# Performance work log

Measured on AMD Instinct MI355X. Metric: run time of the kernel, lower is better.

## Reference

```python
import jax, jax.numpy as jnp
import numpy as np

DIM = 5120
HEADS = 40
HEAD_DIM = DIM // HEADS
EPS = 1e-6


def rms_norm(x, w, eps=EPS):
    var = jnp.mean(jnp.square(x), axis=-1, keepdims=True)
    return x * jax.lax.rsqrt(var + eps) * w


def apply_rotary(x, freqs_cos, freqs_sin):
    # x: [B, L, H, D]; freqs: [1, L, 1, D] (broadcastable)
    x_even = x[..., 0::2]
    x_odd = x[..., 1::2]
    cos_e = freqs_cos[..., 0::2]
    sin_o = freqs_sin[..., 1::2]
    out_even = x_even * cos_e - x_odd * sin_o
    out_odd = x_even * sin_o + x_odd * cos_e
    # interleave back: [..., D//2, 2] -> [..., D]
    return jnp.stack([out_even, out_odd], axis=-1).reshape(x.shape)


def setup_inputs() -> dict:
    key = jax.random.key(0)
    ks = jax.random.split(key, 8)
    B, L = 1, 2048
    scale_in = 1.0 / np.sqrt(DIM)
    return {
        "hidden_states": jax.random.normal(ks[0], (B, L, DIM), jnp.float32),
        "freqs_cos": jax.random.normal(ks[1], (1, L, 1, HEAD_DIM), jnp.float32),
        "freqs_sin": jax.random.normal(ks[2], (1, L, 1, HEAD_DIM), jnp.float32),
        "W_qkv": jax.random.normal(ks[3], (DIM, 3 * DIM), jnp.float32) * scale_in,
        "b_qkv": jnp.zeros((3 * DIM,), jnp.float32),
        "w_norm_q": jnp.ones((DIM,), jnp.float32),
        "w_norm_k": jnp.ones((DIM,), jnp.float32),
        "W_out": jax.random.normal(ks[4], (DIM, DIM), jnp.float32) * scale_in,
        "b_out": jnp.zeros((DIM,), jnp.float32),
    }


def reference(hidden_states, freqs_cos, freqs_sin, W_qkv, b_qkv,
              w_norm_q, w_norm_k, W_out, b_out):
    B, L, D = hidden_states.shape
    qkv = hidden_states @ W_qkv + b_qkv                     # [B, L, 3D]
    q, k, v = jnp.split(qkv, 3, axis=-1)
    q = rms_norm(q, w_norm_q)                               # norm over full dim=5120
    k = rms_norm(k, w_norm_k)
    q = q.reshape(B, L, HEADS, HEAD_DIM)
    k = k.reshape(B, L, HEADS, HEAD_DIM)
    v = v.reshape(B, L, HEADS, HEAD_DIM)
    q = apply_rotary(q, freqs_cos, freqs_sin)
    k = apply_rotary(k, freqs_cos, freqs_sin)
    scale = 1.0 / np.sqrt(HEAD_DIM)
    scores = jnp.einsum("bqhd,bkhd->bhqk", q, k) * scale    # [B, H, L, L]
    attn = jax.nn.softmax(scores, axis=-1)
    out = jnp.einsum("bhqk,bkhd->bqhd", attn, v)            # [B, L, H, D]
    out = out.reshape(B, L, D)
    return out @ W_out + b_out
```

## Files before the change

### kernel.cpp

```cpp
#include <hip/hip_runtime.h>
#include <cstdint>
#include <cstddef>

#define L_C   2048
#define DIMC  5120
#define HD    128
#define NHEADS 40

typedef __bf16 bf16_t;
typedef __bf16 bf16x8 __attribute__((ext_vector_type(8)));
typedef __bf16 bf16x4 __attribute__((ext_vector_type(4)));
typedef float  f32x4  __attribute__((ext_vector_type(4)));

#define MFMA16(A,B,C) __builtin_amdgcn_mfma_f32_16x16x32_bf16((A),(B),(C),0,0,0)
#define BARRIER() __builtin_amdgcn_s_barrier()
#define VMCNT0() asm volatile("s_waitcnt vmcnt(0)" ::: "memory")
#define VMCNT8() asm volatile("s_waitcnt vmcnt(8)" ::: "memory")

__device__ __forceinline__ void gload16(const void* g, void* l) {
  __builtin_amdgcn_global_load_lds(
      (__attribute__((address_space(1))) void*)(void*)g,
      (__attribute__((address_space(3))) void*)l, 16, 0, 0);
}

__global__ __launch_bounds__(256) void f32_to_bf16(const float* __restrict__ in,
                                                   bf16_t* __restrict__ out, size_t n8) {
  size_t i = (size_t)blockIdx.x * blockDim.x + threadIdx.x;
  size_t stride = (size_t)gridDim.x * blockDim.x;
  for (; i < n8; i += stride) {
    f32x4 a = *(const f32x4*)(in + i * 8);
    f32x4 b = *(const f32x4*)(in + i * 8 + 4);
    bf16x8 o;
#pragma unroll
    for (int j = 0; j < 4; ++j) { o[j] = (bf16_t)a[j]; o[4 + j] = (bf16_t)b[j]; }
    *(bf16x8*)(out + i * 8) = o;
  }
}

__global__ __launch_bounds__(256) void wtrans(const float* __restrict__ W,
                                              bf16_t* __restrict__ Wt, int K, int N) {
  __shared__ bf16_t t[64 * 68];
  const int k0 = blockIdx.x * 64, n0 = blockIdx.y * 64, tid = threadIdx.x;
  const int tn = tid & 15, tk = tid >> 4;
  f32x4 v[4];
#pragma unroll
  for (int jj = 0; jj < 4; ++jj)
    v[jj] = *(const f32x4*)(W + (size_t)(k0 + 4 * tk + jj) * N + n0 + 4 * tn);
#pragma unroll
  for (int j = 0; j < 4; ++j) {
    bf16x4 o;
#pragma unroll
    for (int jj = 0; jj < 4; ++jj) o[jj] = (bf16_t)v[jj][j];
    *(bf16x4*)&t[(4 * tn + j) * 68 + 4 * tk] = o;
  }
  __syncthreads();
#pragma unroll
  for (int i = 0; i < 2; ++i) {
    int c = i * 256 + tid, rn = c >> 3, ck = (c & 7) * 8;
    bf16x8 o = *(const bf16x8*)&t[rn * 68 + ck];
    *(bf16x8*)(Wt + (size_t)(n0 + rn) * K + k0 + ck) = o;
  }
}

__global__ __launch_bounds__(256) void v_trans(const bf16_t* __restrict__ qkv,
                                               bf16_t* __restrict__ Vt) {
  __shared__ bf16_t t[128 * 68];
  const int l0 = blockIdx.x * 64, h = blockIdx.y, tid = threadIdx.x;
  const int td = tid & 31, tl = tid >> 5;
#pragma unroll
  for (int it = 0; it < 2; ++it) {
    const int lq = tl + it * 8;
    bf16x4 v[4];
#pragma unroll
    for (int jj = 0; jj < 4; ++jj)
      v[jj] = *(const bf16x4*)(qkv + (size_t)(l0 + 4 * lq + jj) * (3 * DIMC) +
                               2 * DIMC + h * HD + 4 * td);
#pragma unroll
    for (int j = 0; j < 4; ++j) {
      bf16x4 o;
#pragma unroll
      for (int jj = 0; jj < 4; ++jj) o[jj] = v[jj][j];
      *(bf16x4*)&t[(4 * td + j) * 68 + 4 * lq] = o;
    }
  }
  __syncthreads();
#pragma unroll
  for (int i = 0; i < 4; ++i) {
    int c = i * 256 + tid, d = c >> 3, cl = (c & 7) * 8;
    bf16x8 o = *(const bf16x8*)&t[d * 68 + cl];
    *(bf16x8*)(Vt + ((size_t)h * HD + d) * L_C + l0 + cl) = o;
  }
}

template <int OUT_BF16, int K>
__global__ __launch_bounds__(512, 1) void gemm8(const bf16_t* __restrict__ A,
                                                const bf16_t* __restrict__ Bt,
                                                const float* __restrict__ bias,
                                                bf16_t* __restrict__ Cb,
                                                float* __restrict__ Cf,
                                                int M, int N) {
  __shared__ __align__(16) char smem[131072];
  const int tid = threadIdx.x;
  const int wid = tid >> 6, lane = tid & 63;
  const int g = lane >> 4, r = lane & 15;
  const int wm = wid >> 2, wn = wid & 3;
  const int nb = gridDim.x * gridDim.y;
  const int bid = blockIdx.y * gridDim.x + blockIdx.x;
  const int swz = (bid & 7) * (nb >> 3) + (bid >> 3);
  const int bm = swz % gridDim.x, bn = swz / gridDim.x;
  const int row0 = bm * 256, col0 = bn * 256;

  auto stageA = [&](int buf, int half, int kt) {
#pragma unroll
    for (int i = 0; i < 2; ++i) {
      const int idx = i * 512 + tid;
      const int rl = idx >> 3, c = idx & 7;
      gload16(A + (size_t)(row0 + half * 128 + rl) * K + kt * 64 + ((c ^ (rl & 7)) << 3),
              smem + buf * 65536 + half * 16384 + (i * 512 + wid * 64) * 16);
    }
  };
  auto stageB = [&](int buf, int half, int kt) {
#pragma unroll
    for (int i = 0; i < 2; ++i) {
      const int idx = i * 512 + tid;
      const int rl = idx >> 3, c = idx & 7;
      gload16(Bt + (size_t)(col0 + half * 128 + rl) * K + kt * 64 + ((c ^ (rl & 7)) << 3),
              smem + buf * 65536 + 32768 + half * 16384 + (i * 512 + wid * 64) * 16);
    }
  };
  auto ldA = [&](int buf, int mi, int kk) {
    const int rh = mi * 16 + r;
    return *(const bf16x8*)(smem + buf * 65536 + wm * 16384 + rh * 128 +
                            (((kk * 4 + g) ^ (r & 7)) << 4));
  };
  auto ldB = [&](int buf, int ni, int kk) {
    const int rh = (wn & 1) * 64 + ni * 16 + r;
    return *(const bf16x8*)(smem + buf * 65536 + 32768 + (wn >> 1) * 16384 + rh * 128 +
                            (((kk * 4 + g) ^ (r & 7)) << 4));
  };

  f32x4 acc[8][4] = {};
  bf16x8 af[4][2], bfr[4][2];
  constexpr int nk = K / 64;

  stageA(0, 0, 0); stageA(0, 1, 0); stageB(0, 0, 0); stageB(0, 1, 0);
  stageA(1, 0, 1); stageA(1, 1, 1); stageB(1, 0, 1); stageB(1, 1, 1);
  VMCNT8();
  BARRIER();

  auto ktile = [&](int k, int cur) {
    const bool pf2 = (k + 2 < nk);
#pragma unroll
    for (int i = 0; i < 4; ++i)
#pragma unroll
      for (int kk = 0; kk < 2; ++kk) af[i][kk] = ldA(cur, i, kk);
#pragma unroll
    for (int j = 0; j < 2; ++j)
#pragma unroll
      for (int kk = 0; kk < 2; ++kk) bfr[j][kk] = ldB(cur, j, kk);
    BARRIER();
    __builtin_amdgcn_s_setprio(1);
#pragma unroll
    for (int i = 0; i < 4; ++i)
#pragma unroll
      for (int j = 0; j < 2; ++j)
#pragma unroll
        for (int kk = 0; kk < 2; ++kk)
          acc[i][j] = MFMA16(af[i][kk], bfr[j][kk], acc[i][j]);
    __builtin_amdgcn_s_setprio(0);
    BARRIER();
#pragma unroll
    for (int j = 0; j < 2; ++j)
#pragma unroll
      for (int kk = 0; kk < 2; ++kk) bfr[2 + j][kk] = ldB(cur, 2 + j, kk);
    BARRIER();
    __builtin_amdgcn_s_setprio(1);
#pragma unroll
    for (int i = 0; i < 4; ++i)
#pragma unroll
      for (int j = 0; j < 2; ++j)
#pragma unroll
        for (int kk = 0; kk < 2; ++kk)
          acc[i][2 + j] = MFMA16(af[i][kk], bfr[2 + j][kk], acc[i][2 + j]);
    __builtin_amdgcn_s_setprio(0);
    BARRIER();
#pragma unroll
    for (int i = 0; i < 4; ++i)
#pragma unroll
      for (int kk = 0; kk < 2; ++kk) af[i][kk] = ldA(cur, 4 + i, kk);
    if (pf2) { stageB(cur, 0, k + 2); stageB(cur, 1, k + 2); }
    BARRIER();
    __builtin_amdgcn_s_setprio(1);
#pragma unroll
    for (int i = 0; i < 4; ++i)
#pragma unroll
      for (int j = 0; j < 2; ++j)
#pragma unroll
        for (int kk = 0; kk < 2; ++kk)
          acc[4 + i][2 + j] = MFMA16(af[i][kk], bfr[2 + j][kk], acc[4 + i][2 + j]);
    __builtin_amdgcn_s_setprio(0);
    BARRIER();
    if (pf2) { stageA(cur, 0, k + 2); stageA(cur, 1, k + 2); }
    __builtin_amdgcn_s_setprio(1);
#pragma unroll
    for (int i = 0; i < 4; ++i)
#pragma unroll
      for (int j = 0; j < 2; ++j)
#pragma unroll
        for (int kk = 0; kk < 2; ++kk)
          acc[4 + i][j] = MFMA16(af[i][kk], bfr[j][kk], acc[4 + i][j]);
    __builtin_amdgcn_s_setprio(0);
    if (pf2) { VMCNT8(); } else { VMCNT0(); }
    BARRIER();
  };

  for (int kp = 0; kp < nk; kp += 2) { ktile(kp, 0); ktile(kp + 1, 1); }

#pragma unroll
  for (int mi = 0; mi < 8; ++mi)
#pragma unroll
    for (int ni = 0; ni < 4; ++ni)
#pragma unroll
      for (int p = 0; p < 4; ++p) {
        const int rr = row0 + wm * 128 + mi * 16 + 4 * g + p;
        const int cc = col0 + wn * 64 + ni * 16 + r;
        const float v = acc[mi][ni][p] + bias[cc];
        if (OUT_BF16) Cb[(size_t)rr * N + cc] = (bf16_t)v;
        else          Cf[(size_t)rr * N + cc] = v;
      }
}

__global__ __launch_bounds__(256) void norm_rope(const bf16_t* __restrict__ qkv,
                                                 const float* __restrict__ wq,
                                                 const float* __restrict__ wk,
                                                 const float* __restrict__ fcos,
                                                 const float* __restrict__ fsin,
                                                 bf16_t* __restrict__ Qo,
                                                 bf16_t* __restrict__ Ko) {
  __shared__ bf16_t qs[DIMC], ks_[DIMC];
  const int l = blockIdx.x, tid = threadIdx.x;
  const bf16_t* row = qkv + (size_t)l * (3 * DIMC);
  float sq = 0.f, sk = 0.f;
  for (int i = tid; i < DIMC / 8; i += 256) {
    bf16x8 a = *(const bf16x8*)(row + i * 8);
    bf16x8 b = *(const bf16x8*)(row + DIMC + i * 8);
    *(bf16x8*)&qs[i * 8] = a;
    *(bf16x8*)&ks_[i * 8] = b;
#pragma unroll
    for (int j = 0; j < 8; ++j) {
      float x = (float)a[j]; sq += x * x;
      float y = (float)b[j]; sk += y * y;
    }
  }
#pragma unroll
  for (int off = 32; off; off >>= 1) {
    sq += __shfl_xor(sq, off, 64);
    sk += __shfl_xor(sk, off, 64);
  }
  __shared__ float red[2][4];
  const int wid = tid >> 6, lane = tid & 63;
  if (!lane) { red[0][wid] = sq; red[1][wid] = sk; }
  __syncthreads();
  sq = red[0][0] + red[0][1] + red[0][2] + red[0][3];
  sk = red[1][0] + red[1][1] + red[1][2] + red[1][3];
  const float rq = rsqrtf(sq * (1.f / DIMC) + 1e-6f);
  const float rk = rsqrtf(sk * (1.f / DIMC) + 1e-6f);
  for (int i = tid; i < DIMC / 8; i += 256) {
    const int j0 = i * 8, h = j0 >> 7, d0 = j0 & 127;
    bf16x8 a = *(const bf16x8*)&qs[j0];
    bf16x8 b = *(const bf16x8*)&ks_[j0];
    f32x4 cA = *(const f32x4*)(fcos + (size_t)l * HD + d0);
    f32x4 cB = *(const f32x4*)(fcos + (size_t)l * HD + d0 + 4);
    f32x4 sA = *(const f32x4*)(fsin + (size_t)l * HD + d0);
    f32x4 sB = *(const f32x4*)(fsin + (size_t)l * HD + d0 + 4);
    f32x4 wqA = *(const f32x4*)(wq + j0), wqB = *(const f32x4*)(wq + j0 + 4);
    f32x4 wkA = *(const f32x4*)(wk + j0), wkB = *(const f32x4*)(wk + j0 + 4);
    float cc[8], ss[8], qn[8], kn[8];
#pragma unroll
    for (int j = 0; j < 4; ++j) {
      cc[j] = cA[j]; cc[4 + j] = cB[j];
      ss[j] = sA[j]; ss[4 + j] = sB[j];
      qn[j] = (float)a[j] * rq * wqA[j];
      qn[4 + j] = (float)a[4 + j] * rq * wqB[j];
      kn[j] = (float)b[j] * rk * wkA[j];
      kn[4 + j] = (float)b[4 + j] * rk * wkB[j];
    }
    bf16x8 oq, ok;
#pragma unroll
    for (int p = 0; p < 4; ++p) {
      const float c = cc[2 * p], s = ss[2 * p + 1];
      oq[2 * p]     = (bf16_t)(qn[2 * p] * c - qn[2 * p + 1] * s);
      oq[2 * p + 1] = (bf16_t)(qn[2 * p] * s + qn[2 * p + 1] * c);
      ok[2 * p]     = (bf16_t)(kn[2 * p] * c - kn[2 * p + 1] * s);
      ok[2 * p + 1] = (bf16_t)(kn[2 * p] * s + kn[2 * p + 1] * c);
    }
    *(bf16x8*)(Qo + ((size_t)h * L_C + l) * HD + d0) = oq;
    *(bf16x8*)(Ko + ((size_t)h * L_C + l) * HD + d0) = ok;
  }
}

__global__ __launch_bounds__(256, 2) void attn(const bf16_t* __restrict__ Q,
                                               const bf16_t* __restrict__ Kg,
                                               const bf16_t* __restrict__ Vt,
                                               bf16_t* __restrict__ O) {
  __shared__ bf16_t k_lds[64 * HD];
  __shared__ bf16_t v_lds[HD * 64];
  __shared__ bf16_t p_lds[4][2][16 * 72];
  const int tid = threadIdx.x, wid = tid >> 6, lane = tid & 63;
  const int g = lane >> 4, r = lane & 15;
  const int bid = blockIdx.x;
  const int grp = bid & 7, inner = bid >> 3;
  const int h = (inner >> 4) * 8 + grp;
  const int q0 = (inner & 15) * 128 + wid * 32;
  bf16x8 qf[2][4];
#pragma unroll
  for (int rg = 0; rg < 2; ++rg) {
    const bf16_t* qrow = Q + ((size_t)h * L_C + q0 + rg * 16 + r) * HD;
#pragma unroll
    for (int ks = 0; ks < 4; ++ks) qf[rg][ks] = *(const bf16x8*)(qrow + ks * 32 + g * 8);
  }
  f32x4 oacc[2][8] = {};
  float m_i[2][4], l_i[2][4];
#pragma unroll
  for (int rg = 0; rg < 2; ++rg)
#pragma unroll
    for (int p = 0; p < 4; ++p) { m_i[rg][p] = -1e30f; l_i[rg][p] = 0.f; }
  const float scale = 0.08838834764831845f;

  bf16x8 kreg[4], vreg[4];
  auto load_kv = [&](int kv0) {
#pragma unroll
    for (int i = 0; i < 4; ++i) {
      const int c = i * 256 + tid;
      const int krow = c >> 4, kcb = c & 15;
      kreg[i] = *(const bf16x8*)(Kg + ((size_t)h * L_C + kv0 + krow) * HD + kcb * 8);
      const int vrow = c >> 3, vcb = c & 7;
      vreg[i] = *(const bf16x8*)(Vt + ((size_t)h * HD + vrow) * L_C + kv0 + vcb * 8);
    }
  };
  load_kv(0);

  for (int kv0 = 0; kv0 < L_C; kv0 += 64) {
    __syncthreads();
#pragma unroll
    for (int i = 0; i < 4; ++i) {
      const int c = i * 256 + tid;
      const int krow = c >> 4, kcb = c & 15;
      *(bf16x8*)((char*)k_lds + krow * 256 + ((kcb * 16) ^ ((krow & 7) << 4))) = kreg[i];
      const int vrow = c >> 3, vcb = c & 7;
      *(bf16x8*)((char*)v_lds + vrow * 128 + ((vcb * 16) ^ ((vrow & 7) << 4))) = vreg[i];
    }
    if (kv0 + 64 < L_C) load_kv(kv0 + 64);
    __syncthreads();

    float pv[2][4][4];
    __builtin_amdgcn_s_setprio(1);
#pragma unroll
    for (int nf = 0; nf < 4; ++nf) {
      f32x4 s0 = {0.f, 0.f, 0.f, 0.f}, s1 = {0.f, 0.f, 0.f, 0.f};
      const int key = nf * 16 + r;
#pragma unroll
      for (int ks = 0; ks < 4; ++ks) {
        bf16x8 kf = *(const bf16x8*)((const char*)k_lds + key * 256 +
                                     ((ks * 64 + g * 16) ^ ((key & 7) << 4)));
        s0 = MFMA16(qf[0][ks], kf, s0);
        s1 = MFMA16(qf[1][ks], kf, s1);
      }
#pragma unroll
      for (int p = 0; p < 4; ++p) { pv[0][nf][p] = s0[p] * scale; pv[1][nf][p] = s1[p] * scale; }
    }
    __builtin_amdgcn_s_setprio(0);
#pragma unroll
    for (int rg = 0; rg < 2; ++rg) {
      float mnew[4];
#pragma unroll
      for (int p = 0; p < 4; ++p)
        mnew[p] = fmaxf(fmaxf(pv[rg][0][p], pv[rg][1][p]), fmaxf(pv[rg][2][p], pv[rg][3][p]));
#pragma unroll
      for (int m = 1; m < 16; m <<= 1)
#pragma unroll
        for (int p = 0; p < 4; ++p) mnew[p] = fmaxf(mnew[p], __shfl_xor(mnew[p], m, 64));
      float alpha[4], rsum[4];
#pragma unroll
      for (int p = 0; p < 4; ++p) {
        const float mi = fmaxf(m_i[rg][p], mnew[p]);
        alpha[p] = __expf(m_i[rg][p] - mi);
        m_i[rg][p] = mi;
        rsum[p] = 0.f;
      }
#pragma unroll
      for (int nf = 0; nf < 4; ++nf)
#pragma unroll
        for (int p = 0; p < 4; ++p) {
          pv[rg][nf][p] = __expf(pv[rg][nf][p] - m_i[rg][p]);
          rsum[p] += pv[rg][nf][p];
        }
#pragma unroll
      for (int nf = 0; nf < 4; ++nf)
#pragma unroll
        for (int p = 0; p < 4; ++p)
          p_lds[wid][rg][(4 * g + p) * 72 + nf * 16 + r] = (bf16_t)pv[rg][nf][p];
#pragma unroll
      for (int m = 1; m < 16; m <<= 1)
#pragma unroll
        for (int p = 0; p < 4; ++p) rsum[p] += __shfl_xor(rsum[p], m, 64);
#pragma unroll
      for (int p = 0; p < 4; ++p) l_i[rg][p] = l_i[rg][p] * alpha[p] + rsum[p];
#pragma unroll
      for (int nf = 0; nf < 8; ++nf)
#pragma unroll
        for (int p = 0; p < 4; ++p) oacc[rg][nf][p] *= alpha[p];
    }
    bf16x8 pf0[2], pf1[2];
#pragma unroll
    for (int rg = 0; rg < 2; ++rg) {
      pf0[rg] = *(const bf16x8*)&p_lds[wid][rg][r * 72 + 8 * g];
      pf1[rg] = *(const bf16x8*)&p_lds[wid][rg][r * 72 + 32 + 8 * g];
    }
    __builtin_amdgcn_s_setprio(1);
#pragma unroll
    for (int nf = 0; nf < 8; ++nf) {
      const int d = nf * 16 + r;
      bf16x8 vf0 = *(const bf16x8*)((const char*)v_lds + d * 128 +
                                    ((g * 16) ^ ((d & 7) << 4)));
      bf16x8 vf1 = *(const bf16x8*)((const char*)v_lds + d * 128 +
                                    ((64 + g * 16) ^ ((d & 7) << 4)));
#pragma unroll
      for (int rg = 0; rg < 2; ++rg) {
        oacc[rg][nf] = MFMA16(pf0[rg], vf0, oacc[rg][nf]);
        oacc[rg][nf] = MFMA16(pf1[rg], vf1, oacc[rg][nf]);
      }
    }
    __builtin_amdgcn_s_setprio(0);
  }
#pragma unroll
  for (int rg = 0; rg < 2; ++rg)
#pragma unroll
    for (int p = 0; p < 4; ++p) {
      const float inv = 1.f / l_i[rg][p];
      const int rowg = q0 + rg * 16 + 4 * g + p;
#pragma unroll
      for (int nf = 0; nf < 8; ++nf) {
        const int d = nf * 16 + r;
        O[(size_t)rowg * DIMC + h * HD + d] = (bf16_t)(oacc[rg][nf][p] * inv);
      }
    }
}

extern "C" void kernel_launch(void* const* d_in, const int* in_sizes, int n_in,
                              void* d_out, int out_size, void* d_ws, size_t ws_size,
                              hipStream_t stream) {
  const float* hidden = (const float*)d_in[0];
  const float* fcos   = (const float*)d_in[1];
  const float* fsin   = (const float*)d_in[2];
  const float* Wqkv   = (const float*)d_in[3];
  const float* bqkv   = (const float*)d_in[4];
  const float* wnq    = (const float*)d_in[5];
  const float* wnk    = (const float*)d_in[6];
  const float* Wout   = (const float*)d_in[7];
  const float* bout   = (const float*)d_in[8];
  float* out = (float*)d_out;

  char* ws = (char*)d_ws;
  size_t off = 0;
  auto alloc = [&](size_t bytes) {
    void* p = ws + off;
    off += (bytes + 255) & ~(size_t)255;
    return p;
  };
  bf16_t* X   = (bf16_t*)alloc((size_t)L_C * DIMC * 2);
  bf16_t* WQT = (bf16_t*)alloc((size_t)3 * DIMC * DIMC * 2);
  bf16_t* WOT = (bf16_t*)alloc((size_t)DIMC * DIMC * 2);
  bf16_t* QKV = (bf16_t*)alloc((size_t)L_C * 3 * DIMC * 2);
  bf16_t* Qb  = (bf16_t*)alloc((size_t)L_C * DIMC * 2);
  bf16_t* Kb  = (bf16_t*)alloc((size_t)L_C * DIMC * 2);
  bf16_t* VT  = (bf16_t*)alloc((size_t)L_C * DIMC * 2);
  bf16_t* Ob  = X;

  f32_to_bf16<<<2048, 256, 0, stream>>>(hidden, X, (size_t)L_C * DIMC / 8);
  wtrans<<<dim3(DIMC / 64, 3 * DIMC / 64), 256, 0, stream>>>(Wqkv, WQT, DIMC, 3 * DIMC);
  wtrans<<<dim3(DIMC / 64, DIMC / 64), 256, 0, stream>>>(Wout, WOT, DIMC, DIMC);
  gemm8<1, DIMC><<<dim3(L_C / 256, 3 * DIMC / 256), 512, 0, stream>>>(
      X, WQT, bqkv, QKV, nullptr, L_C, 3 * DIMC);
  norm_rope<<<L_C, 256, 0, stream>>>(QKV, wnq, wnk, fcos, fsin, Qb, Kb);
  v_trans<<<dim3(L_C / 64, NHEADS), 256, 0, stream>>>(QKV, VT);
  attn<<<(L_C / 128) * NHEADS, 256, 0, stream>>>(Qb, Kb, VT, Ob);
  gemm8<0, DIMC><<<dim3(L_C / 256, DIMC / 256), 512, 0, stream>>>(
      Ob, WOT, bout, nullptr, out, L_C, DIMC);
}
```

Baseline: 803.8 us.

## Restagger GEMM global-to-LDS prefetches across both k-tiles of the double buffer

```diff
diff --git a/kernel.cpp b/kernel.cpp
--- a/kernel.cpp
+++ b/kernel.cpp
@@ -14,7 +14,10 @@
 
 #define MFMA16(A,B,C) __builtin_amdgcn_mfma_f32_16x16x32_bf16((A),(B),(C),0,0,0)
 #define BARRIER() __builtin_amdgcn_s_barrier()
+#define LGKM0()  asm volatile("s_waitcnt lgkmcnt(0)" ::: "memory")
 #define VMCNT0() asm volatile("s_waitcnt vmcnt(0)" ::: "memory")
+#define VMCNT4() asm volatile("s_waitcnt vmcnt(4)" ::: "memory")
+#define VMCNT6() asm volatile("s_waitcnt vmcnt(6)" ::: "memory")
 #define VMCNT8() asm volatile("s_waitcnt vmcnt(8)" ::: "memory")
 
 __device__ __forceinline__ void gload16(const void* g, void* l) {
@@ -148,73 +151,132 @@
   VMCNT8();
   BARRIER();
 
-  auto ktile = [&](int k, int cur) {
-    const bool pf2 = (k + 2 < nk);
-#pragma unroll
-    for (int i = 0; i < 4; ++i)
-#pragma unroll
-      for (int kk = 0; kk < 2; ++kk) af[i][kk] = ldA(cur, i, kk);
+  for (int t = 0; t < nk; t += 2) {
+    const bool first = (t == 0);
+    const bool pf2 = (t + 2 < nk);
+    const bool pf3 = (t + 3 < nk);
+#pragma unroll
+    for (int i = 0; i < 4; ++i)
+#pragma unroll
+      for (int kk = 0; kk < 2; ++kk) af[i][kk] = ldA(0, i, kk);
 #pragma unroll
     for (int j = 0; j < 2; ++j)
 #pragma unroll
-      for (int kk = 0; kk < 2; ++kk) bfr[j][kk] = ldB(cur, j, kk);
-    BARRIER();
-    __builtin_amdgcn_s_setprio(1);
-#pragma unroll
-    for (int i = 0; i < 4; ++i)
-#pragma unroll
-      for (int j = 0; j < 2; ++j)
-#pragma unroll
-        for (int kk = 0; kk < 2; ++kk)
-          acc[i][j] = MFMA16(af[i][kk], bfr[j][kk], acc[i][j]);
+      for (int kk = 0; kk < 2; ++kk) bfr[j][kk] = ldB(0, j, kk);
+    if (!first) stageA(1, 1, t + 1);
+    BARRIER(); LGKM0();
+    __builtin_amdgcn_s_setprio(1);
+#pragma unroll
+    for (int i = 0; i < 4; ++i)
+#pragma unroll
+      for (int j = 0; j < 2; ++j)
+#pragma unroll
+        for (int kk = 0; kk < 2; ++kk) acc[i][j] = MFMA16(af[i][kk], bfr[j][kk], acc[i][j]);
     __builtin_amdgcn_s_setprio(0);
     BARRIER();
 #pragma unroll
     for (int j = 0; j < 2; ++j)
 #pragma unroll
-      for (int kk = 0; kk < 2; ++kk) bfr[2 + j][kk] = ldB(cur, 2 + j, kk);
-    BARRIER();
-    __builtin_amdgcn_s_setprio(1);
-#pragma unroll
-    for (int i = 0; i < 4; ++i)
-#pragma unroll
-      for (int j = 0; j < 2; ++j)
-#pragma unroll
-        for (int kk = 0; kk < 2; ++kk)
-          acc[i][2 + j] = MFMA16(af[i][kk], bfr[2 + j][kk], acc[i][2 + j]);
-    __builtin_amdgcn_s_setprio(0);
-    BARRIER();
-#pragma unroll
-    for (int i = 0; i < 4; ++i)
-#pragma unroll
-      for (int kk = 0; kk < 2; ++kk) af[i][kk] = ldA(cur, 4 + i, kk);
-    if (pf2) { stageB(cur, 0, k + 2); stageB(cur, 1, k + 2); }
-    BARRIER();
-    __builtin_amdgcn_s_setprio(1);
-#pragma unroll
-    for (int i = 0; i < 4; ++i)
-#pragma unroll
-      for (int j = 0; j < 2; ++j)
-#pragma unroll
-        for (int kk = 0; kk < 2; ++kk)
-          acc[4 + i][2 + j] = MFMA16(af[i][kk], bfr[2 + j][kk], acc[4 + i][2 + j]);
-    __builtin_amdgcn_s_setprio(0);
-    BARRIER();
-    if (pf2) { stageA(cur, 0, k + 2); stageA(cur, 1, k + 2); }
-    __builtin_amdgcn_s_setprio(1);
-#pragma unroll
-    for (int i = 0; i < 4; ++i)
-#pragma unroll
-      for (int j = 0; j < 2; ++j)
-#pragma unroll
-        for (int kk = 0; kk < 2; ++kk)
-          acc[4 + i][j] = MFMA16(af[i][kk], bfr[j][kk], acc[4 + i][j]);
-    __builtin_amdgcn_s_setprio(0);
-    if (pf2) { VMCNT8(); } else { VMCNT0(); }
-    BARRIER();
-  };
-
-  for (int kp = 0; kp < nk; kp += 2) { ktile(kp, 0); ktile(kp + 1, 1); }
+      for (int kk = 0; kk < 2; ++kk) bfr[2 + j][kk] = ldB(0, 2 + j, kk);
+    BARRIER(); LGKM0();
+    __builtin_amdgcn_s_setprio(1);
+#pragma unroll
+    for (int i = 0; i < 4; ++i)
+#pragma unroll
+      for (int j = 0; j < 2; ++j)
+#pragma unroll
+        for (int kk = 0; kk < 2; ++kk) acc[i][2 + j] = MFMA16(af[i][kk], bfr[2 + j][kk], acc[i][2 + j]);
+    __builtin_amdgcn_s_setprio(0);
+    BARRIER();
+#pragma unroll
+    for (int i = 0; i < 4; ++i)
+#pragma unroll
+      for (int kk = 0; kk < 2; ++kk) af[i][kk] = ldA(0, 4 + i, kk);
+    if (pf2) stageB(0, 0, t + 2);
+    BARRIER(); LGKM0();
+    __builtin_amdgcn_s_setprio(1);
+#pragma unroll
+    for (int i = 0; i < 4; ++i)
+#pragma unroll
+      for (int j = 0; j < 2; ++j)
+#pragma unroll
+        for (int kk = 0; kk < 2; ++kk) acc[4 + i][2 + j] = MFMA16(af[i][kk], bfr[2 + j][kk], acc[4 + i][2 + j]);
+    __builtin_amdgcn_s_setprio(0);
+    BARRIER();
+    if (pf2) stageA(0, 0, t + 2);
+    BARRIER();
+    __builtin_amdgcn_s_setprio(1);
+#pragma unroll
+    for (int i = 0; i < 4; ++i)
+#pragma unroll
+      for (int j = 0; j < 2; ++j)
+#pragma unroll
+        for (int kk = 0; kk < 2; ++kk) acc[4 + i][j] = MFMA16(af[i][kk], bfr[j][kk], acc[4 + i][j]);
+    __builtin_amdgcn_s_setprio(0);
+    if (pf2) { VMCNT4(); } else { VMCNT0(); }
+    BARRIER();
+#pragma unroll
+    for (int i = 0; i < 4; ++i)
+#pragma unroll
+      for (int kk = 0; kk < 2; ++kk) af[i][kk] = ldA(1, i, kk);
+#pragma unroll
+    for (int j = 0; j < 2; ++j)
+#pragma unroll
+      for (int kk = 0; kk < 2; ++kk) bfr[j][kk] = ldB(1, j, kk);
+    if (pf2) stageB(0, 1, t + 2);
+    BARRIER(); LGKM0();
+    __builtin_amdgcn_s_setprio(1);
+#pragma unroll
+    for (int i = 0; i < 4; ++i)
+#pragma unroll
+      for (int j = 0; j < 2; ++j)
+#pragma unroll
+        for (int kk = 0; kk < 2; ++kk) acc[i][j] = MFMA16(af[i][kk], bfr[j][kk], acc[i][j]);
+    __builtin_amdgcn_s_setprio(0);
+    BARRIER();
+#pragma unroll
+    for (int j = 0; j < 2; ++j)
+#pragma unroll
+      for (int kk = 0; kk < 2; ++kk) bfr[2 + j][kk] = ldB(1, 2 + j, kk);
+    if (pf2) stageA(0, 1, t + 2);
+    BARRIER(); LGKM0();
+    __builtin_amdgcn_s_setprio(1);
+#pragma unroll
+    for (int i = 0; i < 4; ++i)
+#pragma unroll
+      for (int j = 0; j < 2; ++j)
+#pragma unroll
+        for (int kk = 0; kk < 2; ++kk) acc[i][2 + j] = MFMA16(af[i][kk], bfr[2 + j][kk], acc[i][2 + j]);
+    __builtin_amdgcn_s_setprio(0);
+    BARRIER();
+#pragma unroll
+    for (int i = 0; i < 4; ++i)
+#pragma unroll
+      for (int kk = 0; kk < 2; ++kk) af[i][kk] = ldA(1, 4 + i, kk);
+    if (pf3) stageB(1, 0, t + 3);
+    BARRIER(); LGKM0();
+    __builtin_amdgcn_s_setprio(1);
+#pragma unroll
+    for (int i = 0; i < 4; ++i)
+#pragma unroll
+      for (int j = 0; j < 2; ++j)
+#pragma unroll
+        for (int kk = 0; kk < 2; ++kk) acc[4 + i][2 + j] = MFMA16(af[i][kk], bfr[2 + j][kk], acc[4 + i][2 + j]);
+    __builtin_amdgcn_s_setprio(0);
+    BARRIER();
+    if (pf3) { stageB(1, 1, t + 3); stageA(1, 0, t + 3); }
+    BARRIER();
+    __builtin_amdgcn_s_setprio(1);
+#pragma unroll
+    for (int i = 0; i < 4; ++i)
+#pragma unroll
+      for (int j = 0; j < 2; ++j)
+#pragma unroll
+        for (int kk = 0; kk < 2; ++kk) acc[4 + i][j] = MFMA16(af[i][kk], bfr[j][kk], acc[4 + i][j]);
+    __builtin_amdgcn_s_setprio(0);
+    if (pf2) { VMCNT6(); } else { VMCNT0(); }
+    BARRIER();
+  }
 
 #pragma unroll
   for (int mi = 0; mi < 8; ++mi)
```

New measurement: 777.0 us. 3.3% less time.
